# Kernel tuning notes

Hardware: AMD Instinct MI355X
Metric: run time of the kernel (lower is better)

Reference implementation:

```python
import jax, jax.numpy as jnp
import numpy as np

OBJECTNESS_LIMIT = 0.7
MIN_SIZE = 10.0
N_ANCHORS = 9  # 3 aspects x 3 scales from RPN.anchors


def _conv(x, w, padding):
    return jax.lax.conv_general_dilated(
        x, w, window_strides=(1, 1), padding=padding,
        dimension_numbers=('NHWC', 'HWIO', 'NHWC'))


def setup_inputs() -> dict:
    key = jax.random.key(0)
    ks = jax.random.split(key, 7)
    B, H, W, C = 8, 64, 64, 512
    data = jax.random.normal(ks[0], (B, H, W, C), dtype=jnp.float32)
    # base 3x3 conv 512->256 ('normal' init), relu
    w_base = jax.random.normal(ks[1], (3, 3, C, 256), dtype=jnp.float32) * 0.05
    b_base = jnp.zeros((256,), dtype=jnp.float32)
    # classifier 1x1 conv 256->9 ('uniform' init), sigmoid
    w_cls = jax.random.uniform(ks[2], (1, 1, 256, N_ANCHORS), dtype=jnp.float32,
                               minval=-0.05, maxval=0.05)
    b_cls = jnp.zeros((N_ANCHORS,), dtype=jnp.float32)
    # branch is exercised / gradients flow)
    w_reg = jax.random.normal(ks[3], (1, 1, 256, N_ANCHORS * 4), dtype=jnp.float32) * 0.05
    b_reg = jnp.zeros((N_ANCHORS * 4,), dtype=jnp.float32)
    return {'data': data, 'w_base': w_base, 'b_base': b_base,
            'w_cls': w_cls, 'b_cls': b_cls, 'w_reg': w_reg, 'b_reg': b_reg}


def reference(data, w_base, b_base, w_cls, b_cls, w_reg, b_reg):
    # RPN base conv: 3x3, same padding, relu
    feat = jax.nn.relu(_conv(data, w_base, 'SAME') + b_base)        # [B,H,W,256]
    obj = jax.nn.sigmoid(_conv(feat, w_cls, 'VALID') + b_cls)       # [B,H,W,9]
    boxes = _conv(feat, w_reg, 'VALID') + b_reg                     # [B,H,W,36]
    B, H, W, _ = boxes.shape
    boxes = boxes.reshape(B, H, W, N_ANCHORS, 4)
    mask = (obj > OBJECTNESS_LIMIT) & (boxes[..., 2] > MIN_SIZE) & (boxes[..., 3] > MIN_SIZE)
    # boxes failing selection are dropped (yielded as None) -> zeroed here
    boxes = jnp.where(mask[..., None], boxes, jnp.zeros((), boxes.dtype))
    # objectness is always emitted; pack (boxes, objectness) densely
    out = jnp.concatenate([boxes.reshape(B, H, W, N_ANCHORS * 4), obj], axis=-1)  # [B,H,W,45]
    return out
```

## Files before the change

### kernel.cpp

```cpp
#include <hip/hip_runtime.h>
#include <hip/hip_bf16.h>

typedef unsigned short u16;
typedef unsigned int   u32;

typedef __attribute__((ext_vector_type(8))) short bfrag;
typedef __attribute__((ext_vector_type(4))) float f32x4;

static __device__ __forceinline__ u16 f2bf(float f) {
    u32 u = __float_as_uint(f);
    return (u16)((u + 0x7fffu + ((u >> 16) & 1u)) >> 16);
}
static __device__ __forceinline__ u32 pk2(float a, float b) {
    return (u32)f2bf(a) | ((u32)f2bf(b) << 16);
}
static __device__ __forceinline__ float bf2f(u16 h) {
    return __uint_as_float((u32)h << 16);
}

#define AS1 __attribute__((address_space(1)))
#define AS3 __attribute__((address_space(3)))
static __device__ __forceinline__ void gload_lds16(const u16* g, u16* l) {
    __builtin_amdgcn_global_load_lds((const AS1 u32*)g, (AS3 u32*)l, 16, 0, 0);
}

__global__ __launch_bounds__(256) void prep_all_k(
    const float* __restrict__ data,
    const float* __restrict__ wb,
    const float* __restrict__ wc,
    const float* __restrict__ wr,
    u16* __restrict__ abf,
    u16* __restrict__ wt,
    u16* __restrict__ wh)
{
    int b = blockIdx.x, tid = threadIdx.x;
    if (b < 8712) {
        int gid = b * 256 + tid;
        int ch8 = gid & 63;
        int row = gid >> 6;
        int img = row / 4356;
        int rem = row - img * 4356;
        int py  = rem / 66;
        int px  = rem - py * 66;
        uint4 o;
        if (py == 0 || py == 65 || px == 0 || px == 65) {
            o = make_uint4(0u, 0u, 0u, 0u);
        } else {
            const float4* s = (const float4*)(data +
                ((size_t)((img << 12) + ((py - 1) << 6) + (px - 1)) << 9) + (ch8 << 3));
            float4 v0 = s[0], v1 = s[1];
            o = make_uint4(pk2(v0.x, v0.y), pk2(v0.z, v0.w),
                           pk2(v1.x, v1.y), pk2(v1.z, v1.w));
        }
        *(uint4*)(abf + ((size_t)row << 9) + (ch8 << 3)) = o;
    } else if (b < 13320) {
        int i  = (b - 8712) * 256 + tid;
        int ci = i & 511;
        int co = (i >> 9) & 255;
        int pos = i >> 17;
        wt[i] = f2bf(wb[(size_t)((pos << 9) + ci) * 256 + co]);
    } else {
        int i = (b - 13320) * 256 + tid;
        int ch = i >> 8, c = i & 255;
        float v = 0.f;
        if (ch < 36)      v = wr[c * 36 + ch];
        else if (ch < 45) v = wc[c * 9 + ch - 36];
        wh[i] = f2bf(v);
    }
}

__global__ __launch_bounds__(256, 2) void gemm_k(
    const u16*   __restrict__ abf,
    const u16*   __restrict__ wt,
    const float* __restrict__ bb,
    u16*         __restrict__ feat)
{
    __shared__ u16 As[128 * 128];
    __shared__ u16 Bs[128 * 128];

    int bid = blockIdx.x;
    int wg  = ((bid & 7) << 6) | (bid >> 3);
    int mt  = wg >> 1, nt = wg & 1;
    int pm0 = mt << 7, cn0 = nt << 7;
    int img = mt >> 5;
    int y0  = (mt & 31) << 1;

    int tid = threadIdx.x, lane = tid & 63, w = tid >> 6;
    int wm2 = (w >> 1) << 6, wn2 = (w & 1) << 6;
    int fr = lane & 15, fg = lane >> 4;

    const u16* pA[8]; const u16* pB[8];
    int ldsOff[8];
    #pragma unroll
    for (int i = 0; i < 8; ++i) {
        int slot = i * 256 + w * 64 + lane;
        int row  = slot >> 4, g = slot & 15;
        int gs   = g ^ (row & 7);
        int y = y0 + (row >> 6), x = row & 63;
        pA[i] = abf + ((size_t)((img * 66 + y) * 66 + x) << 9) + (gs << 3);
        pB[i] = wt  + ((size_t)(cn0 + row) << 9) + (gs << 3);
        ldsOff[i] = (i * 256 + w * 64) << 3;
    }

    int aoff[4][4], boff[4][4];
    #pragma unroll
    for (int kk = 0; kk < 4; ++kk)
        #pragma unroll
        for (int t = 0; t < 4; ++t) {
            int ra = wm2 + (t << 4) + fr;
            int rb = wn2 + (t << 4) + fr;
            int q  = (kk << 2) | fg;
            aoff[kk][t] = (ra << 7) + ((q ^ (ra & 7)) << 3);
            boff[kk][t] = (rb << 7) + ((q ^ (rb & 7)) << 3);
        }

    f32x4 acc[4][4] = {};

    #pragma unroll 1
    for (int kb = 0; kb < 4; ++kb) {
        size_t kOff = (size_t)(kb << 7);
        #pragma unroll 1
        for (int pos = 0; pos < 9; ++pos) {
            int py = pos / 3, px = pos % 3;
            size_t soA = (((size_t)(py * 66 + px)) << 9) + kOff;
            size_t soB = (((size_t)pos) << 17) + kOff;
            #pragma unroll
            for (int i = 0; i < 8; ++i) gload_lds16(pA[i] + soA, &As[ldsOff[i]]);
            #pragma unroll
            for (int i = 0; i < 8; ++i) gload_lds16(pB[i] + soB, &Bs[ldsOff[i]]);
            __syncthreads();

            #pragma unroll
            for (int kk = 0; kk < 4; ++kk) {
                bfrag av[4], bv[4];
                #pragma unroll
                for (int t = 0; t < 4; ++t) {
                    av[t] = *(const bfrag*)&As[aoff[kk][t]];
                    bv[t] = *(const bfrag*)&Bs[boff[kk][t]];
                }
                #pragma unroll
                for (int mi = 0; mi < 4; ++mi)
                    #pragma unroll
                    for (int ni = 0; ni < 4; ++ni)
                        acc[mi][ni] = __builtin_amdgcn_mfma_f32_16x16x32_bf16(
                            av[mi], bv[ni], acc[mi][ni], 0, 0, 0);
            }
            __syncthreads();
        }
    }

    #pragma unroll
    for (int ni = 0; ni < 4; ++ni) {
        int co = cn0 + wn2 + (ni << 4) + fr;
        float bias = bb[co];
        #pragma unroll
        for (int mi = 0; mi < 4; ++mi) {
            int pixb = pm0 + wm2 + (mi << 4) + (fg << 2);
            #pragma unroll
            for (int r = 0; r < 4; ++r) {
                float v = fmaxf(acc[mi][ni][r] + bias, 0.f);
                feat[(size_t)(pixb + r) * 256 + co] = f2bf(v);
            }
        }
    }
}

__global__ __launch_bounds__(256, 2) void head_k(
    const u16*   __restrict__ feat,
    const u16*   __restrict__ wh,
    const float* __restrict__ bc,
    const float* __restrict__ br,
    float*       __restrict__ out)
{
    __shared__ union {
        u16   ft[64 * 256];
        float raw[64 * 45];
    } sm;

    int bid = blockIdx.x;
    int wg  = ((bid & 7) << 6) | (bid >> 3);
    int pb  = wg << 6;

    int tid = threadIdx.x, lane = tid & 63, w = tid >> 6;
    int fr = lane & 15, fg = lane >> 4;
    int wm = w << 4;

    bfrag bv[3][8];
    #pragma unroll
    for (int nt = 0; nt < 3; ++nt)
        #pragma unroll
        for (int kk = 0; kk < 8; ++kk)
            bv[nt][kk] = *(const bfrag*)(wh + ((nt << 4) + fr) * 256 + (kk << 5) + (fg << 3));

    const u16* fbase = feat + ((size_t)pb << 8);
    #pragma unroll
    for (int i = 0; i < 8; ++i) {
        int slot = i * 256 + tid;
        int row  = slot >> 5, g = slot & 31;
        int gs   = g ^ (row & 7);
        gload_lds16(fbase + (row << 8) + (gs << 3), &sm.ft[(i * 256 + w * 64) << 3]);
    }
    __syncthreads();

    f32x4 acc[3] = {};
    #pragma unroll
    for (int kk = 0; kk < 8; ++kk) {
        int row = wm + fr;
        int ga  = (kk << 2) | fg;
        bfrag av = *(const bfrag*)&sm.ft[(row << 8) + ((ga ^ (row & 7)) << 3)];
        #pragma unroll
        for (int nt = 0; nt < 3; ++nt)
            acc[nt] = __builtin_amdgcn_mfma_f32_16x16x32_bf16(av, bv[nt][kk], acc[nt], 0, 0, 0);
    }
    __syncthreads();

    #pragma unroll
    for (int nt = 0; nt < 3; ++nt) {
        int ch = (nt << 4) + fr;
        if (ch < 45) {
            float bias = (ch < 36) ? br[ch] : bc[ch - 36];
            int pix = wm + (fg << 2);
            #pragma unroll
            for (int r = 0; r < 4; ++r)
                sm.raw[(pix + r) * 45 + ch] = acc[nt][r] + bias;
        }
    }
    __syncthreads();

    {
        int pix = tid >> 2, q = tid & 3;
        const float* rp = &sm.raw[pix * 45];
        float* op = out + (size_t)(pb + pix) * 45;
        int na = (q == 3) ? 3 : 2;
        int a0 = (q == 3) ? 6 : (q << 1);
        for (int t = 0; t < na; ++t) {
            int a = a0 + t;
            float lg  = rp[36 + a];
            float obj = 1.f / (1.f + __expf(-lg));
            float b0 = rp[4*a], b1 = rp[4*a+1], b2 = rp[4*a+2], b3 = rp[4*a+3];
            bool m = (obj > 0.7f) && (b2 > 10.f) && (b3 > 10.f);
            op[4*a    ] = m ? b0 : 0.f;
            op[4*a + 1] = m ? b1 : 0.f;
            op[4*a + 2] = m ? b2 : 0.f;
            op[4*a + 3] = m ? b3 : 0.f;
            op[36 + a ] = obj;
        }
    }
}

__global__ __launch_bounds__(256) void prep_w_k(const float* __restrict__ wb,
                                                u16* __restrict__ wt)
{
    int i  = blockIdx.x * 256 + threadIdx.x;
    int ci = i & 511;
    int co = (i >> 9) & 255;
    int pos = i >> 17;
    wt[i] = f2bf(wb[(size_t)((pos << 9) + ci) * 256 + co]);
}

union FbSmem {
    u16   hal[3 * 66 * 64];
    u16   ft[256][64];
    float raw[64 * 45];
};

template<int WMODE>
__global__ __launch_bounds__(256, 2) void fb_k(
    const float* __restrict__ data, const u16* __restrict__ wt,
    const float* __restrict__ wb, const float* __restrict__ bb,
    const float* __restrict__ wc, const float* __restrict__ bc,
    const float* __restrict__ wr, const float* __restrict__ br,
    float* __restrict__ out)
{
    __shared__ FbSmem sm;
    int bid = blockIdx.x;
    int wg  = ((bid & 7) << 6) | (bid >> 3);
    int pm0 = wg << 6;
    int img = wg >> 6;
    int y0  = wg & 63;
    int tid = threadIdx.x, lane = tid & 63, wid = tid >> 6;
    int wn = wid << 6;
    int fr = lane & 15, fg = lane >> 4;
    f32x4 acc[4][4] = {};

    #pragma unroll 1
    for (int cb = 0; cb < 8; ++cb) {
        __syncthreads();
        #pragma unroll
        for (int t = 0; t < 3; ++t) {
            int lin = t * 256 + tid;
            int row = lin >> 8, col = (lin >> 2) & 63, cq = lin & 3;
            int sy = y0 + row - 1;
            bool ok = (sy >= 0) && (sy < 64);
            float4 v0, v1, v2, v3;
            if (ok) {
                const float4* s = (const float4*)(data +
                    ((size_t)((img << 12) + (sy << 6) + col) << 9) + (cb << 6) + (cq << 4));
                v0 = s[0]; v1 = s[1]; v2 = s[2]; v3 = s[3];
            } else { v0 = v1 = v2 = v3 = make_float4(0.f, 0.f, 0.f, 0.f); }
            int hc = col + 1;
            u16* base = &sm.hal[(row * 66 + hc) << 6];
            int g0 = ((cq << 1) | 0) ^ (hc & 7);
            int g1 = ((cq << 1) | 1) ^ (hc & 7);
            *(uint4*)&base[g0 << 3] = make_uint4(pk2(v0.x,v0.y), pk2(v0.z,v0.w),
                                                 pk2(v1.x,v1.y), pk2(v1.z,v1.w));
            *(uint4*)&base[g1 << 3] = make_uint4(pk2(v2.x,v2.y), pk2(v2.z,v2.w),
                                                 pk2(v3.x,v3.y), pk2(v3.z,v3.w));
        }
        if (tid < 48) {
            int zr = tid >> 4, zrem = tid & 15;
            int zc = (zrem >> 3) ? 65 : 0, zg = zrem & 7;
            *(uint4*)&sm.hal[(((zr * 66 + zc) << 3) | zg) << 3] = make_uint4(0,0,0,0);
        }
        __syncthreads();

        #pragma unroll
        for (int pos = 0; pos < 9; ++pos) {
            int dy = pos / 3 - 1, dx = pos % 3 - 1;
            bfrag bv[2][4];
            if (WMODE == 0) {
                #pragma unroll
                for (int kk = 0; kk < 2; ++kk)
                    #pragma unroll
                    for (int i = 0; i < 4; ++i)
                        bv[kk][i] = *(const bfrag*)(wt + ((size_t)pos << 17) +
                            ((size_t)(wn + (i << 4) + fr) << 9) + (cb << 6) +
                            (kk << 5) + (fg << 3));
            } else {
                #pragma unroll
                for (int kk = 0; kk < 2; ++kk)
                    #pragma unroll
                    for (int i = 0; i < 4; ++i) {
                        int co = wn + (i << 4) + fr;
                        const float* s = wb +
                            (size_t)((pos << 9) + (cb << 6) + (kk << 5) + (fg << 3)) * 256 + co;
                        union { short sh[8]; bfrag v; } tb;
                        #pragma unroll
                        for (int j = 0; j < 8; ++j) tb.sh[j] = (short)f2bf(s[(size_t)j << 8]);
                        bv[kk][i] = tb.v;
                    }
            }
            int hr = dy + 1;
            bfrag av[2][4];
            #pragma unroll
            for (int kk = 0; kk < 2; ++kk)
                #pragma unroll
                for (int i = 0; i < 4; ++i) {
                    int hc = (i << 4) + fr + dx + 1;
                    int g  = ((kk << 2) | fg) ^ (hc & 7);
                    av[kk][i] = *(const bfrag*)&sm.hal[(((hr * 66 + hc) << 3) | g) << 3];
                }
            #pragma unroll
            for (int kk = 0; kk < 2; ++kk)
                #pragma unroll
                for (int mi = 0; mi < 4; ++mi)
                    #pragma unroll
                    for (int ni = 0; ni < 4; ++ni)
                        acc[mi][ni] = __builtin_amdgcn_mfma_f32_16x16x32_bf16(
                            av[kk][mi], bv[kk][ni], acc[mi][ni], 0, 0, 0);
        }
    }
    __syncthreads();

    #pragma unroll
    for (int ni = 0; ni < 4; ++ni) {
        int co = wn + (ni << 4) + fr;
        float bias = bb[co];
        int rot = (co & 15) << 2;
        #pragma unroll
        for (int mi = 0; mi < 4; ++mi) {
            int pb  = (mi << 4) + (fg << 2);
            int col = (pb + rot) & 63;
            float r0 = fmaxf(acc[mi][ni][0] + bias, 0.f);
            float r1 = fmaxf(acc[mi][ni][1] + bias, 0.f);
            float r2 = fmaxf(acc[mi][ni][2] + bias, 0.f);
            float r3 = fmaxf(acc[mi][ni][3] + bias, 0.f);
            *(uint2*)&sm.ft[co][col] = make_uint2(pk2(r0, r1), pk2(r2, r3));
        }
    }
    __syncthreads();

    int wchx = __builtin_amdgcn_readfirstlane(wid) * 12;
    float a12[12];
    #pragma unroll
    for (int j = 0; j < 12; ++j) {
        int ch = wchx + j;
        a12[j] = (ch < 36) ? br[ch] : ((ch < 45) ? bc[ch - 36] : 0.f);
    }
    #pragma unroll 4
    for (int c = 0; c < 256; ++c) {
        int col = (lane + ((c & 15) << 2)) & 63;
        float f = bf2f(sm.ft[c][col]);
        #pragma unroll
        for (int j = 0; j < 12; ++j) {
            int ch = wchx + j;
            if (ch < 36)      a12[j] = fmaf(f, wr[c * 36 + ch], a12[j]);
            else if (ch < 45) a12[j] = fmaf(f, wc[c * 9 + ch - 36], a12[j]);
        }
    }
    __syncthreads();
    #pragma unroll
    for (int j = 0; j < 12; ++j) {
        int ch = wchx + j;
        if (ch < 45) sm.raw[lane * 45 + ch] = a12[j];
    }
    __syncthreads();
    {
        int pix = tid >> 2, q = tid & 3;
        const float* rp = &sm.raw[pix * 45];
        float* op = out + (size_t)(pm0 + pix) * 45;
        int na = (q == 3) ? 3 : 2;
        int a0 = (q == 3) ? 6 : (q << 1);
        for (int t = 0; t < na; ++t) {
            int a = a0 + t;
            float lg  = rp[36 + a];
            float obj = 1.f / (1.f + __expf(-lg));
            float b0 = rp[4*a], b1 = rp[4*a+1], b2 = rp[4*a+2], b3 = rp[4*a+3];
            bool m = (obj > 0.7f) && (b2 > 10.f) && (b3 > 10.f);
            op[4*a    ] = m ? b0 : 0.f;
            op[4*a + 1] = m ? b1 : 0.f;
            op[4*a + 2] = m ? b2 : 0.f;
            op[4*a + 3] = m ? b3 : 0.f;
            op[36 + a ] = obj;
        }
    }
}

extern "C" void kernel_launch(void* const* d_in, const int* in_sizes, int n_in,
                              void* d_out, int out_size, void* d_ws, size_t ws_size,
                              hipStream_t stream)
{
    const float* data = (const float*)d_in[0];
    const float* wb   = (const float*)d_in[1];
    const float* bb   = (const float*)d_in[2];
    const float* wc   = (const float*)d_in[3];
    const float* bcl  = (const float*)d_in[4];
    const float* wr   = (const float*)d_in[5];
    const float* brg  = (const float*)d_in[6];
    float* out = (float*)d_out;

    const size_t ABF_B  = (size_t)8 * 66 * 66 * 512 * 2;
    const size_t WT_B   = (size_t)9 * 256 * 512 * 2;
    const size_t FEAT_B = (size_t)32768 * 256 * 2;
    const size_t WH_B   = (size_t)64 * 256 * 2;

    if (ws_size >= ABF_B + WT_B + FEAT_B + WH_B) {
        u16* abf  = (u16*)d_ws;
        u16* wt   = (u16*)((char*)d_ws + ABF_B);
        u16* feat = (u16*)((char*)d_ws + ABF_B + WT_B);
        u16* wh   = (u16*)((char*)d_ws + ABF_B + WT_B + FEAT_B);
        prep_all_k<<<13384, 256, 0, stream>>>(data, wb, wc, wr, abf, wt, wh);
        gemm_k<<<512, 256, 0, stream>>>(abf, wt, bb, feat);
        head_k<<<512, 256, 0, stream>>>(feat, wh, bcl, brg, out);
    } else if (ws_size >= WT_B) {
        u16* wt = (u16*)d_ws;
        prep_w_k<<<4608, 256, 0, stream>>>(wb, wt);
        fb_k<0><<<512, 256, 0, stream>>>(data, wt, wb, bb, wc, bcl, wr, brg, out);
    } else {
        fb_k<1><<<512, 256, 0, stream>>>(data, (const u16*)nullptr, wb,
                                         bb, wc, bcl, wr, brg, out);
    }
}
```

Before: 105.9 us.

## Double-buffer LDS tiles with K=64 stages to overlap loads and MFMA

Result: slower. 110.2 us (+4.1%).

```diff
diff --git a/kernel.cpp b/kernel.cpp
--- a/kernel.cpp
+++ b/kernel.cpp
@@ -75,8 +75,8 @@
     const float* __restrict__ bb,
     u16*         __restrict__ feat)
 {
-    __shared__ u16 As[128 * 128];
-    __shared__ u16 Bs[128 * 128];
+    __shared__ u16 As[2][128 * 64];
+    __shared__ u16 Bs[2][128 * 64];
 
     int bid = blockIdx.x;
     int wg  = ((bid & 7) << 6) | (bid >> 3);
@@ -89,12 +89,12 @@
     int wm2 = (w >> 1) << 6, wn2 = (w & 1) << 6;
     int fr = lane & 15, fg = lane >> 4;
 
-    const u16* pA[8]; const u16* pB[8];
-    int ldsOff[8];
-    #pragma unroll
-    for (int i = 0; i < 8; ++i) {
+    const u16* pA[4]; const u16* pB[4];
+    int ldsOff[4];
+    #pragma unroll
+    for (int i = 0; i < 4; ++i) {
         int slot = i * 256 + w * 64 + lane;
-        int row  = slot >> 4, g = slot & 15;
+        int row  = slot >> 3, g = slot & 7;
         int gs   = g ^ (row & 7);
         int y = y0 + (row >> 6), x = row & 63;
         pA[i] = abf + ((size_t)((img * 66 + y) * 66 + x) << 9) + (gs << 3);
@@ -102,51 +102,64 @@
         ldsOff[i] = (i * 256 + w * 64) << 3;
     }
 
-    int aoff[4][4], boff[4][4];
-    #pragma unroll
-    for (int kk = 0; kk < 4; ++kk)
+    int aoff[2][4], boff[2][4];
+    #pragma unroll
+    for (int kk = 0; kk < 2; ++kk)
         #pragma unroll
         for (int t = 0; t < 4; ++t) {
             int ra = wm2 + (t << 4) + fr;
             int rb = wn2 + (t << 4) + fr;
             int q  = (kk << 2) | fg;
-            aoff[kk][t] = (ra << 7) + ((q ^ (ra & 7)) << 3);
-            boff[kk][t] = (rb << 7) + ((q ^ (rb & 7)) << 3);
+            aoff[kk][t] = (ra << 6) + ((q ^ (ra & 7)) << 3);
+            boff[kk][t] = (rb << 6) + ((q ^ (rb & 7)) << 3);
         }
 
     f32x4 acc[4][4] = {};
 
+    auto stage = [&](int s, int buf) {
+        int kb  = s / 18;
+        int rem = s - kb * 18;
+        int pos = rem >> 1;
+        int py  = pos / 3, px = pos - py * 3;
+        size_t ko  = ((size_t)kb << 7) + ((size_t)(rem & 1) << 6);
+        size_t soA = (((size_t)(py * 66 + px)) << 9) + ko;
+        size_t soB = (((size_t)pos) << 17) + ko;
+        u16* ad = &As[buf][0];
+        u16* bd = &Bs[buf][0];
+        #pragma unroll
+        for (int i = 0; i < 4; ++i) gload_lds16(pA[i] + soA, ad + ldsOff[i]);
+        #pragma unroll
+        for (int i = 0; i < 4; ++i) gload_lds16(pB[i] + soB, bd + ldsOff[i]);
+    };
+    auto compute = [&](int buf) {
+        const u16* a = &As[buf][0];
+        const u16* b = &Bs[buf][0];
+        #pragma unroll
+        for (int kk = 0; kk < 2; ++kk) {
+            bfrag av[4], bv[4];
+            #pragma unroll
+            for (int t = 0; t < 4; ++t) {
+                av[t] = *(const bfrag*)(a + aoff[kk][t]);
+                bv[t] = *(const bfrag*)(b + boff[kk][t]);
+            }
+            #pragma unroll
+            for (int mi = 0; mi < 4; ++mi)
+                #pragma unroll
+                for (int ni = 0; ni < 4; ++ni)
+                    acc[mi][ni] = __builtin_amdgcn_mfma_f32_16x16x32_bf16(
+                        av[mi], bv[ni], acc[mi][ni], 0, 0, 0);
+        }
+    };
+
+    stage(0, 0);
+    __syncthreads();
+    int cur = 0;
     #pragma unroll 1
-    for (int kb = 0; kb < 4; ++kb) {
-        size_t kOff = (size_t)(kb << 7);
-        #pragma unroll 1
-        for (int pos = 0; pos < 9; ++pos) {
-            int py = pos / 3, px = pos % 3;
-            size_t soA = (((size_t)(py * 66 + px)) << 9) + kOff;
-            size_t soB = (((size_t)pos) << 17) + kOff;
-            #pragma unroll
-            for (int i = 0; i < 8; ++i) gload_lds16(pA[i] + soA, &As[ldsOff[i]]);
-            #pragma unroll
-            for (int i = 0; i < 8; ++i) gload_lds16(pB[i] + soB, &Bs[ldsOff[i]]);
-            __syncthreads();
-
-            #pragma unroll
-            for (int kk = 0; kk < 4; ++kk) {
-                bfrag av[4], bv[4];
-                #pragma unroll
-                for (int t = 0; t < 4; ++t) {
-                    av[t] = *(const bfrag*)&As[aoff[kk][t]];
-                    bv[t] = *(const bfrag*)&Bs[boff[kk][t]];
-                }
-                #pragma unroll
-                for (int mi = 0; mi < 4; ++mi)
-                    #pragma unroll
-                    for (int ni = 0; ni < 4; ++ni)
-                        acc[mi][ni] = __builtin_amdgcn_mfma_f32_16x16x32_bf16(
-                            av[mi], bv[ni], acc[mi][ni], 0, 0, 0);
-            }
-            __syncthreads();
-        }
+    for (int s = 0; s < 72; ++s) {
+        if (s < 71) stage(s + 1, cur ^ 1);
+        compute(cur);
+        __syncthreads();
+        cur ^= 1;
     }
 
     #pragma unroll
```
